# Performance work log

Measured on AMD Instinct MI355X. Metric: run time of the kernel, lower is better.

Reference implementation:

```python
import jax, jax.numpy as jnp
import numpy as np

T, N, E, IN_DIM, H = 20, 50000, 800000, 16, 128
NPF = 7  # num_physical_features
EPS = 1e-5


def setup_inputs() -> dict:
    key = jax.random.key(0)
    ks = jax.random.split(key, 24)
    s = 0.05
    inp = {
        'x': jax.random.normal(ks[0], (T, N, IN_DIM), jnp.float32),
        'edge_index': jax.random.randint(ks[1], (2, E), 0, N, jnp.int64),
        # SAGEConv layer 1 (PyG: lin_l on aggregated neighbors w/ bias, lin_r on root no bias)
        'sage1_wl': jax.random.normal(ks[2], (IN_DIM, H), jnp.float32) * s,
        'sage1_bl': jnp.zeros((H,), jnp.float32),
        'sage1_wr': jax.random.normal(ks[3], (IN_DIM, H), jnp.float32) * s,
        # SAGEConv layer 2
        'sage2_wl': jax.random.normal(ks[4], (H, H), jnp.float32) * s,
        'sage2_bl': jnp.zeros((H,), jnp.float32),
        'sage2_wr': jax.random.normal(ks[5], (H, H), jnp.float32) * s,
        # LayerNorm
        'ln_g': jnp.ones((H,), jnp.float32),
        'ln_b': jnp.zeros((H,), jnp.float32),
        # GRU (torch layout: [3H, H], gate order r,z,n)
        'gru_wih': jax.random.normal(ks[6], (3 * H, H), jnp.float32) * s,
        'gru_whh': jax.random.normal(ks[7], (3 * H, H), jnp.float32) * s,
        'gru_bih': jnp.zeros((3 * H,), jnp.float32),
        'gru_bhh': jnp.zeros((3 * H,), jnp.float32),
        # Thickness decoder
        'th_w1': jax.random.normal(ks[8], (H, H), jnp.float32) * s,
        'th_b1': jnp.zeros((H,), jnp.float32),
        'th_w2': jax.random.normal(ks[9], (H, 1), jnp.float32) * s,
        'th_b2': jnp.zeros((1,), jnp.float32),
        # Physical feature decoder
        'ph_w1': jax.random.normal(ks[10], (H, H), jnp.float32) * s,
        'ph_b1': jnp.zeros((H,), jnp.float32),
        'ph_w2': jax.random.normal(ks[11], (H, NPF), jnp.float32) * s,
        'ph_b2': jnp.zeros((NPF,), jnp.float32),
    }
    return inp


def _sage(h, src, dst, deg_inv, wl, bl, wr):
    # mean-aggregate neighbor features over incoming edges, then two linears
    agg = jax.ops.segment_sum(h[src], dst, num_segments=N) * deg_inv[:, None]
    return agg @ wl + bl + h @ wr


def _forward(x, edge_index,
             sage1_wl, sage1_bl, sage1_wr,
             sage2_wl, sage2_bl, sage2_wr,
             ln_g, ln_b,
             gru_wih, gru_whh, gru_bih, gru_bhh,
             th_w1, th_b1, th_w2, th_b2,
             ph_w1, ph_b1, ph_w2, ph_b2):
    src, dst = edge_index[0], edge_index[1]
    deg = jax.ops.segment_sum(jnp.ones((E,), jnp.float32), dst, num_segments=N)
    deg_inv = 1.0 / jnp.maximum(deg, 1.0)

    def encode(xt):  # [N, IN_DIM] -> [N, H]
        h = jax.nn.relu(_sage(xt, src, dst, deg_inv, sage1_wl, sage1_bl, sage1_wr))
        h = jax.nn.relu(_sage(h, src, dst, deg_inv, sage2_wl, sage2_bl, sage2_wr))
        mu = jnp.mean(h, axis=-1, keepdims=True)
        var = jnp.mean(jnp.square(h - mu), axis=-1, keepdims=True)
        return (h - mu) * jax.lax.rsqrt(var + EPS) * ln_g + ln_b

    encoded = jax.lax.map(encode, x)  # [T, N, H]

    # GRU over time, batch = nodes
    def gru_step(h, x_t):
        gi = x_t @ gru_wih.T + gru_bih  # [N, 3H]
        gh = h @ gru_whh.T + gru_bhh
        i_r, i_z, i_n = jnp.split(gi, 3, axis=-1)
        h_r, h_z, h_n = jnp.split(gh, 3, axis=-1)
        r = jax.nn.sigmoid(i_r + h_r)
        z = jax.nn.sigmoid(i_z + h_z)
        n = jnp.tanh(i_n + r * h_n)
        h_new = (1.0 - z) * n + z * h
        return h_new, h_new

    h0 = jnp.zeros((N, H), jnp.float32)
    _, h_temporal = jax.lax.scan(gru_step, h0, encoded)  # [T, N, H]

    th = jax.nn.relu(h_temporal @ th_w1 + th_b1) @ th_w2 + th_b2   # [T, N, 1]
    ph = jax.nn.relu(h_temporal @ ph_w1 + ph_b1) @ ph_w2 + ph_b2   # [T, N, NPF]
    return th, ph


def reference(x, edge_index,
              sage1_wl, sage1_bl, sage1_wr,
              sage2_wl, sage2_bl, sage2_wr,
              ln_g, ln_b,
              gru_wih, gru_whh, gru_bih, gru_bhh,
              th_w1, th_b1, th_w2, th_b2,
              ph_w1, ph_b1, ph_w2, ph_b2):
    return _forward(x, edge_index,
                    sage1_wl, sage1_bl, sage1_wr,
                    sage2_wl, sage2_bl, sage2_wr,
                    ln_g, ln_b,
                    gru_wih, gru_whh, gru_bih, gru_bhh,
                    th_w1, th_b1, th_w2, th_b2,
                    ph_w1, ph_b1, ph_w2, ph_b2)
```

## Files before the change

### kernel.cpp

```cpp
#include <hip/hip_runtime.h>
#include <hip/hip_bf16.h>

#define TT 20
#define NN 50000
#define EE 800000
#define IND 16
#define HH 128
#define NPF 7
#define NB ((NN + 255) / 256)

typedef __attribute__((ext_vector_type(8))) short bf16x8;
typedef __attribute__((ext_vector_type(4))) float f32x4;
#define MFMA(a, b, c) __builtin_amdgcn_mfma_f32_16x16x32_bf16(a, b, c, 0, 0, 0)

__device__ __forceinline__ unsigned short f2bf(float f) {
    union { float f; unsigned u; } v; v.f = f;
    unsigned r = v.u + 0x7fffu + ((v.u >> 16) & 1u);
    return (unsigned short)(r >> 16);
}
__device__ __forceinline__ float bf2f(unsigned short u) {
    union { unsigned u; float f; } v; v.u = ((unsigned)u) << 16;
    return v.f;
}

__global__ void detect_kernel(const int* ei, int* flag, int E) {
    __shared__ int nz;
    if (threadIdx.x == 0) nz = 0;
    __syncthreads();
    for (int i = threadIdx.x; i < 1024 && i < E; i += blockDim.x)
        if (ei[2 * i + 1] != 0) atomicOr(&nz, 1);
    __syncthreads();
    if (threadIdx.x == 0) *flag = (nz == 0) ? 1 : 0;
}
__device__ __forceinline__ int edge_src(const int* ei, int e, int E, int f) {
    return f ? ei[2 * e] : ei[e];
}
__device__ __forceinline__ int edge_dst(const int* ei, int e, int E, int f) {
    return f ? ei[2 * (E + e)] : ei[E + e];
}
__global__ void count_deg_kernel(const int* ei, const int* flag, int* deg, int E) {
    int e = blockIdx.x * blockDim.x + threadIdx.x;
    if (e >= E) return;
    int f = *flag;
    atomicAdd(&deg[edge_dst(ei, e, E, f)], 1);
}

__global__ __launch_bounds__(256) void sum_blocks_kernel(const int* deg, int* bsum) {
    int i = blockIdx.x * 256 + threadIdx.x;
    int v = (i < NN) ? deg[i] : 0;
#pragma unroll
    for (int o = 1; o <= 32; o <<= 1) v += __shfl_xor(v, o);
    __shared__ int ws[4];
    if ((threadIdx.x & 63) == 0) ws[threadIdx.x >> 6] = v;
    __syncthreads();
    if (threadIdx.x == 0) bsum[blockIdx.x] = ws[0] + ws[1] + ws[2] + ws[3];
}
__global__ __launch_bounds__(256) void scan_blocks_kernel(const int* bsum, int* bbase) {
    __shared__ int arr[256];
    int t = threadIdx.x;
    int v = (t < NB) ? bsum[t] : 0;
    arr[t] = v;
    __syncthreads();
    for (int off = 1; off < 256; off <<= 1) {
        int u = (t >= off) ? arr[t - off] : 0;
        __syncthreads();
        arr[t] += u;
        __syncthreads();
    }
    if (t < NB) bbase[t] = arr[t] - v;
}
__global__ __launch_bounds__(256) void offs_kernel(const int* deg, const int* bbase,
                                                   int* offs, int* cursor,
                                                   float* dinv, int E) {
    __shared__ int arr[256];
    int t = threadIdx.x;
    int i = blockIdx.x * 256 + t;
    int d = (i < NN) ? deg[i] : 0;
    arr[t] = d;
    __syncthreads();
    for (int off = 1; off < 256; off <<= 1) {
        int u = (t >= off) ? arr[t - off] : 0;
        __syncthreads();
        arr[t] += u;
        __syncthreads();
    }
    if (i < NN) {
        int o = bbase[blockIdx.x] + arr[t] - d;
        offs[i] = o;
        cursor[i] = o;
        dinv[i] = 1.0f / (float)(d > 1 ? d : 1);
        if (i == NN - 1) offs[NN] = E;
    }
}
__global__ void fill_csr_kernel(const int* ei, const int* flag, int* cursor,
                                int* csr, int E) {
    int e = blockIdx.x * blockDim.x + threadIdx.x;
    if (e >= E) return;
    int f = *flag;
    int s = edge_src(ei, e, E, f);
    int d = edge_dst(ei, e, E, f);
    int p = atomicAdd(&cursor[d], 1);
    csr[p] = s;
}

__global__ void pack_kernel(const float* src, unsigned short* dst, int tiles,
                            int mode) {
    int id = blockIdx.x * blockDim.x + threadIdx.x;
    if (id >= tiles * 4 * 64) return;
    int lane = id & 63, kk = (id >> 6) & 3, tile = id >> 8;
    int n = tile * 16 + (lane & 15);
    int kbase = kk * 32 + (lane >> 4) * 8;
    unsigned short out[8];
#pragma unroll
    for (int i = 0; i < 8; ++i) {
        int k = kbase + i;
        float v = mode ? src[n * HH + k] : src[k * (tiles * 16) + n];
        out[i] = f2bf(v);
    }
    *(uint4*)(dst + (size_t)id * 8) = *(uint4*)out;
}

__global__ __launch_bounds__(128) void sage1_kernel(
    const float* __restrict__ x, const int* __restrict__ offs,
    const int* __restrict__ csr, const float* __restrict__ dinv,
    const float* __restrict__ wl, const float* __restrict__ bl,
    const float* __restrict__ wr, unsigned short* __restrict__ h1c, int t0) {
    const int tid = threadIdx.x;
    const int ci = blockIdx.y;
    const float* xt = x + (size_t)(t0 + ci) * NN * IND;
    const int m0 = blockIdx.x * 8;
    __shared__ __align__(16) float sAgg[8][IND];
    __shared__ float sX[8][IND];
    {
        int r = tid >> 4, node = m0 + r;
        int l16 = tid & 15, sub = l16 >> 2, q = l16 & 3;
        int e1 = offs[node + 1];
        float4 acc = make_float4(0.f, 0.f, 0.f, 0.f);
        for (int e = offs[node] + sub; e < e1; e += 4) {
            float4 v = *(const float4*)(xt + (size_t)csr[e] * IND + q * 4);
            acc.x += v.x; acc.y += v.y; acc.z += v.z; acc.w += v.w;
        }
#pragma unroll
        for (int o = 4; o <= 8; o <<= 1) {
            acc.x += __shfl_xor(acc.x, o);
            acc.y += __shfl_xor(acc.y, o);
            acc.z += __shfl_xor(acc.z, o);
            acc.w += __shfl_xor(acc.w, o);
        }
        if (sub == 0) {
            float di = dinv[node];
            acc.x *= di; acc.y *= di; acc.z *= di; acc.w *= di;
            *(float4*)&sAgg[r][q * 4] = acc;
        }
        sX[r][l16] = xt[(size_t)node * IND + l16];
    }
    __syncthreads();
    const int col = tid;
    float acc[8];
    float b = bl[col];
#pragma unroll
    for (int m = 0; m < 8; ++m) acc[m] = b;
#pragma unroll
    for (int k = 0; k < IND; ++k) {
        float wlv = wl[k * HH + col];
        float wrv = wr[k * HH + col];
#pragma unroll
        for (int m = 0; m < 8; ++m) acc[m] += sAgg[m][k] * wlv + sX[m][k] * wrv;
    }
#pragma unroll
    for (int m = 0; m < 8; ++m)
        h1c[((size_t)ci * NN + m0 + m) * HH + col] = f2bf(fmaxf(acc[m], 0.f));
}

__global__ __launch_bounds__(256) void sage2_agg_kernel(
    const unsigned short* __restrict__ h1c, const int* __restrict__ offs,
    const int* __restrict__ csr, const float* __restrict__ dinv,
    unsigned short* __restrict__ agg2c) {
    const int ci = blockIdx.y;
    const unsigned short* h1t = h1c + (size_t)ci * NN * HH;
    int wid = threadIdx.x >> 6, lane = threadIdx.x & 63;
    int n = blockIdx.x * 4 + wid;
    int eg = lane >> 4, part = lane & 15;
    int e0 = offs[n], e1 = offs[n + 1];
    float s[8] = {0.f, 0.f, 0.f, 0.f, 0.f, 0.f, 0.f, 0.f};
    for (int e = e0 + eg; e < e1; e += 4) {
        uint4 v = *(const uint4*)(h1t + (size_t)csr[e] * HH + part * 8);
        s[0] += bf2f((unsigned short)(v.x & 0xffff));
        s[1] += bf2f((unsigned short)(v.x >> 16));
        s[2] += bf2f((unsigned short)(v.y & 0xffff));
        s[3] += bf2f((unsigned short)(v.y >> 16));
        s[4] += bf2f((unsigned short)(v.z & 0xffff));
        s[5] += bf2f((unsigned short)(v.z >> 16));
        s[6] += bf2f((unsigned short)(v.w & 0xffff));
        s[7] += bf2f((unsigned short)(v.w >> 16));
    }
#pragma unroll
    for (int j = 0; j < 8; ++j) {
        s[j] += __shfl_xor(s[j], 16);
        s[j] += __shfl_xor(s[j], 32);
    }
    if (eg == 0) {
        float di = dinv[n];
        unsigned short o[8];
#pragma unroll
        for (int j = 0; j < 8; ++j) o[j] = f2bf(s[j] * di);
        *(uint4*)(agg2c + ((size_t)ci * NN + n) * HH + part * 8) = *(uint4*)o;
    }
}

#define LDA(buf, kk)                                                          \
    (*(const bf16x8*)((const char*)(buf) +                                    \
        (((lane & 15) * 256 + (kk) * 64 + (lane >> 4) * 16) ^                 \
         (((lane & 15) & 7) << 4))))

__global__ __launch_bounds__(64) void gru_fused_kernel(
    const unsigned short* __restrict__ agg2t, const unsigned short* __restrict__ h1t,
    const unsigned short* __restrict__ pS2L, const unsigned short* __restrict__ pS2R,
    const float* __restrict__ s2bl, const float* __restrict__ lng,
    const float* __restrict__ lnb,
    const unsigned short* __restrict__ pGI, const unsigned short* __restrict__ pGH,
    const float* __restrict__ bih, const float* __restrict__ bhh,
    float* __restrict__ h, unsigned short* __restrict__ hallt) {
    const int lane = threadIdx.x;
    const int r0 = blockIdx.x * 16;
    __shared__ unsigned short bufA[16 * 128];
    __shared__ unsigned short bufB[16 * 128];
    __shared__ unsigned short bufH[16 * 128];

#pragma unroll
    for (int j = 0; j < 4; ++j) {
        int off = (lane + 64 * j) * 16;
        int row = off >> 8;
        int swz = off ^ ((row & 7) << 4);
        *(uint4*)((char*)bufA + swz) =
            *(const uint4*)((const char*)(agg2t + (size_t)r0 * HH) + off);
        *(uint4*)((char*)bufB + swz) =
            *(const uint4*)((const char*)(h1t + (size_t)r0 * HH) + off);
        const float* hs = h + (size_t)r0 * HH + (size_t)(off / 2);
        unsigned short tmp[8];
#pragma unroll
        for (int i = 0; i < 8; ++i) tmp[i] = f2bf(hs[i]);
        *(uint4*)((char*)bufH + swz) = *(uint4*)tmp;
    }
    __syncthreads();

    bf16x8 ae[4], ah[4];
#pragma unroll
    for (int kk = 0; kk < 4; ++kk) { ae[kk] = LDA(bufA, kk); ah[kk] = LDA(bufB, kk); }
    float vE[8][4];
    float sS[4] = {0, 0, 0, 0}, sQ[4] = {0, 0, 0, 0};
#pragma unroll
    for (int c = 0; c < 8; ++c) {
        f32x4 al = {0, 0, 0, 0}, ar = {0, 0, 0, 0};
#pragma unroll
        for (int kk = 0; kk < 4; ++kk) {
            bf16x8 bl = *(const bf16x8*)(pS2L + ((size_t)(c * 4 + kk) * 64 + lane) * 8);
            bf16x8 br = *(const bf16x8*)(pS2R + ((size_t)(c * 4 + kk) * 64 + lane) * 8);
            al = MFMA(ae[kk], bl, al);
            ar = MFMA(ah[kk], br, ar);
        }
        int col = c * 16 + (lane & 15);
        float bb = s2bl[col];
#pragma unroll
        for (int j = 0; j < 4; ++j) {
            float v = fmaxf(al[j] + ar[j] + bb, 0.f);
            vE[c][j] = v; sS[j] += v; sQ[j] += v * v;
        }
    }
#pragma unroll
    for (int o = 1; o <= 8; o <<= 1) {
#pragma unroll
        for (int j = 0; j < 4; ++j) {
            sS[j] += __shfl_xor(sS[j], o);
            sQ[j] += __shfl_xor(sQ[j], o);
        }
    }
    __syncthreads();
#pragma unroll
    for (int c = 0; c < 8; ++c) {
        int col = c * 16 + (lane & 15);
        float g = lng[col], b = lnb[col];
#pragma unroll
        for (int j = 0; j < 4; ++j) {
            float mu = sS[j] * (1.f / 128.f);
            float var = sQ[j] * (1.f / 128.f) - mu * mu;
            float ve = (vE[c][j] - mu) * rsqrtf(var + 1e-5f) * g + b;
            int row = (lane >> 4) * 4 + j;
            int off = ((row * 128 + col) * 2) ^ ((row & 7) << 4);
            *(unsigned short*)((char*)bufA + off) = f2bf(ve);
        }
    }
    __syncthreads();

    bf16x8 xe[4], xh[4];
#pragma unroll
    for (int kk = 0; kk < 4; ++kk) { xe[kk] = LDA(bufA, kk); xh[kk] = LDA(bufH, kk); }
#pragma unroll
    for (int c = 0; c < 8; ++c) {
        f32x4 air = {0,0,0,0}, aiz = {0,0,0,0}, ain = {0,0,0,0};
        f32x4 ahr = {0,0,0,0}, ahz = {0,0,0,0}, ahn = {0,0,0,0};
#pragma unroll
        for (int kk = 0; kk < 4; ++kk) {
            bf16x8 bir = *(const bf16x8*)(pGI + ((size_t)((c     ) * 4 + kk) * 64 + lane) * 8);
            bf16x8 biz = *(const bf16x8*)(pGI + ((size_t)((c +  8) * 4 + kk) * 64 + lane) * 8);
            bf16x8 bin = *(const bf16x8*)(pGI + ((size_t)((c + 16) * 4 + kk) * 64 + lane) * 8);
            bf16x8 bhr = *(const bf16x8*)(pGH + ((size_t)((c     ) * 4 + kk) * 64 + lane) * 8);
            bf16x8 bhz = *(const bf16x8*)(pGH + ((size_t)((c +  8) * 4 + kk) * 64 + lane) * 8);
            bf16x8 bhn = *(const bf16x8*)(pGH + ((size_t)((c + 16) * 4 + kk) * 64 + lane) * 8);
            air = MFMA(xe[kk], bir, air); aiz = MFMA(xe[kk], biz, aiz);
            ain = MFMA(xe[kk], bin, ain);
            ahr = MFMA(xh[kk], bhr, ahr); ahz = MFMA(xh[kk], bhz, ahz);
            ahn = MFMA(xh[kk], bhn, ahn);
        }
        int col = c * 16 + (lane & 15);
        float bir_ = bih[col], biz_ = bih[HH + col], bin_ = bih[2 * HH + col];
        float bhr_ = bhh[col], bhz_ = bhh[HH + col], bhn_ = bhh[2 * HH + col];
#pragma unroll
        for (int j = 0; j < 4; ++j) {
            int row = (lane >> 4) * 4 + j;
            size_t gidx = (size_t)(r0 + row) * HH + col;
            float rr = 1.f / (1.f + expf(-(air[j] + bir_ + ahr[j] + bhr_)));
            float zz = 1.f / (1.f + expf(-(aiz[j] + biz_ + ahz[j] + bhz_)));
            float nn2 = tanhf(ain[j] + bin_ + rr * (ahn[j] + bhn_));
            float hold = h[gidx];
            float hnew = (1.f - zz) * nn2 + zz * hold;
            h[gidx] = hnew;
            hallt[gidx] = f2bf(hnew);
        }
    }
}

__global__ __launch_bounds__(64) void dec_kernel(
    const unsigned short* __restrict__ hall,
    const unsigned short* __restrict__ pT1, const unsigned short* __restrict__ pP1,
    const float* __restrict__ tb1, const float* __restrict__ tw2,
    const float* __restrict__ tb2, const float* __restrict__ pb1,
    const float* __restrict__ pw2, const float* __restrict__ pb2,
    float* __restrict__ out_th, float* __restrict__ out_ph, int t0) {
    const int lane = threadIdx.x;
    const int rc = blockIdx.x * 16;
    const int ci = rc / NN;
    const int n0 = rc - ci * NN;
    const int tg = t0 + ci;
    __shared__ unsigned short bufB[16 * 128];
#pragma unroll
    for (int j = 0; j < 4; ++j) {
        int off = (lane + 64 * j) * 16;
        int row = off >> 8;
        int swz = off ^ ((row & 7) << 4);
        *(uint4*)((char*)bufB + swz) =
            *(const uint4*)((const char*)(hall + (size_t)rc * HH) + off);
    }
    __syncthreads();
    bf16x8 xd[4];
#pragma unroll
    for (int kk = 0; kk < 4; ++kk) xd[kk] = LDA(bufB, kk);
    float pt[4] = {0, 0, 0, 0};
    float pf[NPF][4];
#pragma unroll
    for (int f = 0; f < NPF; ++f)
#pragma unroll
        for (int j = 0; j < 4; ++j) pf[f][j] = 0.f;
#pragma unroll
    for (int c = 0; c < 8; ++c) {
        f32x4 at = {0, 0, 0, 0}, ap = {0, 0, 0, 0};
#pragma unroll
        for (int kk = 0; kk < 4; ++kk) {
            bf16x8 bt = *(const bf16x8*)(pT1 + ((size_t)(c * 4 + kk) * 64 + lane) * 8);
            bf16x8 bp = *(const bf16x8*)(pP1 + ((size_t)(c * 4 + kk) * 64 + lane) * 8);
            at = MFMA(xd[kk], bt, at);
            ap = MFMA(xd[kk], bp, ap);
        }
        int col = c * 16 + (lane & 15);
        float b1 = tb1[col], b2 = pb1[col], w2 = tw2[col];
        float wp[NPF];
#pragma unroll
        for (int f = 0; f < NPF; ++f) wp[f] = pw2[col * NPF + f];
#pragma unroll
        for (int j = 0; j < 4; ++j) {
            float a = fmaxf(at[j] + b1, 0.f);
            pt[j] += a * w2;
            float p = fmaxf(ap[j] + b2, 0.f);
#pragma unroll
            for (int f = 0; f < NPF; ++f) pf[f][j] += p * wp[f];
        }
    }
#pragma unroll
    for (int o = 1; o <= 8; o <<= 1) {
#pragma unroll
        for (int j = 0; j < 4; ++j) {
            pt[j] += __shfl_xor(pt[j], o);
#pragma unroll
            for (int f = 0; f < NPF; ++f) pf[f][j] += __shfl_xor(pf[f][j], o);
        }
    }
    if ((lane & 15) == 0) {
        int g = lane >> 4;
#pragma unroll
        for (int j = 0; j < 4; ++j) {
            int gr = n0 + g * 4 + j;
            out_th[(size_t)tg * NN + gr] = pt[j] + tb2[0];
#pragma unroll
            for (int f = 0; f < NPF; ++f)
                out_ph[((size_t)tg * NN + gr) * NPF + f] = pf[f][j] + pb2[f];
        }
    }
}
#undef LDA

extern "C" void kernel_launch(void* const* d_in, const int* in_sizes, int n_in,
                              void* d_out, int out_size, void* d_ws, size_t ws_size,
                              hipStream_t stream) {
    const float* x     = (const float*)d_in[0];
    const int*   ei    = (const int*)d_in[1];
    const float* s1wl  = (const float*)d_in[2];
    const float* s1bl  = (const float*)d_in[3];
    const float* s1wr  = (const float*)d_in[4];
    const float* s2wl  = (const float*)d_in[5];
    const float* s2bl  = (const float*)d_in[6];
    const float* s2wr  = (const float*)d_in[7];
    const float* lng   = (const float*)d_in[8];
    const float* lnb   = (const float*)d_in[9];
    const float* g_wih = (const float*)d_in[10];
    const float* g_whh = (const float*)d_in[11];
    const float* g_bih = (const float*)d_in[12];
    const float* g_bhh = (const float*)d_in[13];
    const float* tw1   = (const float*)d_in[14];
    const float* tb1   = (const float*)d_in[15];
    const float* tw2   = (const float*)d_in[16];
    const float* tb2   = (const float*)d_in[17];
    const float* pw1   = (const float*)d_in[18];
    const float* pb1   = (const float*)d_in[19];
    const float* pw2   = (const float*)d_in[20];
    const float* pb2   = (const float*)d_in[21];

    char* ws = (char*)d_ws;
    size_t o = 0;
    auto alloc = [&](size_t bytes) {
        size_t r = o;
        o += (bytes + 255) & ~(size_t)255;
        return r;
    };
    int*            flag  = (int*)(ws + alloc(4));
    int*            deg   = (int*)(ws + alloc((size_t)NN * 4));
    int*            offs  = (int*)(ws + alloc((size_t)(NN + 1) * 4));
    int*            curs  = (int*)(ws + alloc((size_t)NN * 4));
    int*            csr   = (int*)(ws + alloc((size_t)EE * 4));
    float*          dinv  = (float*)(ws + alloc((size_t)NN * 4));
    int*            bsum  = (int*)(ws + alloc((size_t)NB * 4));
    int*            bbase = (int*)(ws + alloc((size_t)NB * 4));
    unsigned short* pS2L  = (unsigned short*)(ws + alloc(8 * 4 * 64 * 8 * 2));
    unsigned short* pS2R  = (unsigned short*)(ws + alloc(8 * 4 * 64 * 8 * 2));
    unsigned short* pT1   = (unsigned short*)(ws + alloc(8 * 4 * 64 * 8 * 2));
    unsigned short* pP1   = (unsigned short*)(ws + alloc(8 * 4 * 64 * 8 * 2));
    unsigned short* pGI   = (unsigned short*)(ws + alloc(24 * 4 * 64 * 8 * 2));
    unsigned short* pGH   = (unsigned short*)(ws + alloc(24 * 4 * 64 * 8 * 2));
    float*          hbuf  = (float*)(ws + alloc((size_t)NN * HH * 4));

    const size_t per_t = 2ull * NN * HH * 2;
    size_t avail = (o < ws_size) ? ws_size - o : 0;
    int C = (int)(avail / per_t);
    if (C < 1) C = 1;
    if (C > TT) C = TT;
    unsigned short* h1c   = (unsigned short*)(ws + alloc((size_t)C * NN * HH * 2));
    unsigned short* agg2c = (unsigned short*)(ws + alloc((size_t)C * NN * HH * 2));
    unsigned short* hallc = agg2c;

    detect_kernel<<<1, 256, 0, stream>>>(ei, flag, EE);
    hipMemsetAsync(deg, 0, (size_t)NN * 4, stream);
    count_deg_kernel<<<(EE + 255) / 256, 256, 0, stream>>>(ei, flag, deg, EE);
    sum_blocks_kernel<<<NB, 256, 0, stream>>>(deg, bsum);
    scan_blocks_kernel<<<1, 256, 0, stream>>>(bsum, bbase);
    offs_kernel<<<NB, 256, 0, stream>>>(deg, bbase, offs, curs, dinv, EE);
    fill_csr_kernel<<<(EE + 255) / 256, 256, 0, stream>>>(ei, flag, curs, csr, EE);
    pack_kernel<<<(8 * 4 * 64 + 255) / 256, 256, 0, stream>>>(s2wl, pS2L, 8, 0);
    pack_kernel<<<(8 * 4 * 64 + 255) / 256, 256, 0, stream>>>(s2wr, pS2R, 8, 0);
    pack_kernel<<<(8 * 4 * 64 + 255) / 256, 256, 0, stream>>>(tw1, pT1, 8, 0);
    pack_kernel<<<(8 * 4 * 64 + 255) / 256, 256, 0, stream>>>(pw1, pP1, 8, 0);
    pack_kernel<<<(24 * 4 * 64 + 255) / 256, 256, 0, stream>>>(g_wih, pGI, 24, 1);
    pack_kernel<<<(24 * 4 * 64 + 255) / 256, 256, 0, stream>>>(g_whh, pGH, 24, 1);
    hipMemsetAsync(hbuf, 0, (size_t)NN * HH * 4, stream);

    float* out = (float*)d_out;
    for (int t0 = 0; t0 < TT; t0 += C) {
        int Cc = TT - t0 < C ? TT - t0 : C;
        dim3 g1(NN / 8, Cc), g2(NN / 4, Cc);
        sage1_kernel<<<g1, 128, 0, stream>>>(x, offs, csr, dinv, s1wl, s1bl,
                                             s1wr, h1c, t0);
        sage2_agg_kernel<<<g2, 256, 0, stream>>>(h1c, offs, csr, dinv, agg2c);
        for (int ci = 0; ci < Cc; ++ci) {
            size_t co = (size_t)ci * NN * HH;
            gru_fused_kernel<<<NN / 16, 64, 0, stream>>>(
                agg2c + co, h1c + co, pS2L, pS2R, s2bl, lng, lnb, pGI, pGH,
                g_bih, g_bhh, hbuf, hallc + co);
        }
        dec_kernel<<<(size_t)Cc * NN / 16, 64, 0, stream>>>(
            hallc, pT1, pP1, tb1, tw2, tb2, pb1, pw2, pb2,
            out, out + (size_t)TT * NN, t0);
    }
}
```

Measured before the change: 2.691 ms.

## Restructure sage2 aggregation, process two row tiles per GRU block, drop LDS staging

The sage2 aggregation now assigns 16 lanes per node, with 4-way unrolled independent gathers and no cross-lane reduction. The fused GRU kernel handles 32 rows per block so each packed weight fragment feeds two MFMA tiles. MFMA A-fragments are loaded straight from global memory instead of being staged through swizzled LDS, in both the GRU and decoder kernels. The csr index read in sage1 uses a nontemporal load. These changes add register pressure from the doubled accumulators and make the fragment loads less coalesced.

```diff
diff --git a/kernel.cpp b/kernel.cpp
--- a/kernel.cpp
+++ b/kernel.cpp
@@ -137,7 +137,8 @@
         int e1 = offs[node + 1];
         float4 acc = make_float4(0.f, 0.f, 0.f, 0.f);
         for (int e = offs[node] + sub; e < e1; e += 4) {
-            float4 v = *(const float4*)(xt + (size_t)csr[e] * IND + q * 4);
+            int s = __builtin_nontemporal_load(&csr[e]);
+            float4 v = *(const float4*)(xt + (size_t)s * IND + q * 4);
             acc.x += v.x; acc.y += v.y; acc.z += v.z; acc.w += v.w;
         }
 #pragma unroll
@@ -172,46 +173,49 @@
         h1c[((size_t)ci * NN + m0 + m) * HH + col] = f2bf(fmaxf(acc[m], 0.f));
 }
 
+#define ADD8(acc, v) do {                                     \
+    union { unsigned u; float f; } t_;                        \
+    t_.u = (v).x << 16;         acc[0] += t_.f;               \
+    t_.u = (v).x & 0xffff0000u; acc[1] += t_.f;               \
+    t_.u = (v).y << 16;         acc[2] += t_.f;               \
+    t_.u = (v).y & 0xffff0000u; acc[3] += t_.f;               \
+    t_.u = (v).z << 16;         acc[4] += t_.f;               \
+    t_.u = (v).z & 0xffff0000u; acc[5] += t_.f;               \
+    t_.u = (v).w << 16;         acc[6] += t_.f;               \
+    t_.u = (v).w & 0xffff0000u; acc[7] += t_.f;               \
+} while (0)
+
 __global__ __launch_bounds__(256) void sage2_agg_kernel(
     const unsigned short* __restrict__ h1c, const int* __restrict__ offs,
     const int* __restrict__ csr, const float* __restrict__ dinv,
     unsigned short* __restrict__ agg2c) {
     const int ci = blockIdx.y;
-    const unsigned short* h1t = h1c + (size_t)ci * NN * HH;
-    int wid = threadIdx.x >> 6, lane = threadIdx.x & 63;
-    int n = blockIdx.x * 4 + wid;
-    int eg = lane >> 4, part = lane & 15;
-    int e0 = offs[n], e1 = offs[n + 1];
-    float s[8] = {0.f, 0.f, 0.f, 0.f, 0.f, 0.f, 0.f, 0.f};
-    for (int e = e0 + eg; e < e1; e += 4) {
-        uint4 v = *(const uint4*)(h1t + (size_t)csr[e] * HH + part * 8);
-        s[0] += bf2f((unsigned short)(v.x & 0xffff));
-        s[1] += bf2f((unsigned short)(v.x >> 16));
-        s[2] += bf2f((unsigned short)(v.y & 0xffff));
-        s[3] += bf2f((unsigned short)(v.y >> 16));
-        s[4] += bf2f((unsigned short)(v.z & 0xffff));
-        s[5] += bf2f((unsigned short)(v.z >> 16));
-        s[6] += bf2f((unsigned short)(v.w & 0xffff));
-        s[7] += bf2f((unsigned short)(v.w >> 16));
-    }
-#pragma unroll
-    for (int j = 0; j < 8; ++j) {
-        s[j] += __shfl_xor(s[j], 16);
-        s[j] += __shfl_xor(s[j], 32);
-    }
-    if (eg == 0) {
-        float di = dinv[n];
-        unsigned short o[8];
-#pragma unroll
-        for (int j = 0; j < 8; ++j) o[j] = f2bf(s[j] * di);
-        *(uint4*)(agg2c + ((size_t)ci * NN + n) * HH + part * 8) = *(uint4*)o;
-    }
-}
-
-#define LDA(buf, kk)                                                          \
-    (*(const bf16x8*)((const char*)(buf) +                                    \
-        (((lane & 15) * 256 + (kk) * 64 + (lane >> 4) * 16) ^                 \
-         (((lane & 15) & 7) << 4))))
+    const unsigned short* __restrict__ h1t = h1c + (size_t)ci * NN * HH;
+    const int n = blockIdx.x * 16 + (threadIdx.x >> 4);
+    const int part = threadIdx.x & 15;
+    const int e0 = offs[n], e1 = offs[n + 1];
+    float a[8] = {0,0,0,0,0,0,0,0}, b[8] = {0,0,0,0,0,0,0,0};
+    float c_[8] = {0,0,0,0,0,0,0,0}, d[8] = {0,0,0,0,0,0,0,0};
+    int e = e0;
+    for (; e + 3 < e1; e += 4) {
+        int s0 = csr[e], s1 = csr[e + 1], s2 = csr[e + 2], s3 = csr[e + 3];
+        uint4 v0 = *(const uint4*)(h1t + (size_t)s0 * HH + part * 8);
+        uint4 v1 = *(const uint4*)(h1t + (size_t)s1 * HH + part * 8);
+        uint4 v2 = *(const uint4*)(h1t + (size_t)s2 * HH + part * 8);
+        uint4 v3 = *(const uint4*)(h1t + (size_t)s3 * HH + part * 8);
+        ADD8(a, v0); ADD8(b, v1); ADD8(c_, v2); ADD8(d, v3);
+    }
+    for (; e < e1; ++e) {
+        int s0 = csr[e];
+        uint4 v0 = *(const uint4*)(h1t + (size_t)s0 * HH + part * 8);
+        ADD8(a, v0);
+    }
+    float di = dinv[n];
+    unsigned short o[8];
+#pragma unroll
+    for (int j = 0; j < 8; ++j) o[j] = f2bf((a[j] + b[j] + c_[j] + d[j]) * di);
+    *(uint4*)(agg2c + ((size_t)ci * NN + n) * HH + part * 8) = *(uint4*)o;
+}
 
 __global__ __launch_bounds__(64) void gru_fused_kernel(
     const unsigned short* __restrict__ agg2t, const unsigned short* __restrict__ h1t,
@@ -222,83 +226,89 @@
     const float* __restrict__ bih, const float* __restrict__ bhh,
     float* __restrict__ h, unsigned short* __restrict__ hallt) {
     const int lane = threadIdx.x;
-    const int r0 = blockIdx.x * 16;
-    __shared__ unsigned short bufA[16 * 128];
-    __shared__ unsigned short bufB[16 * 128];
-    __shared__ unsigned short bufH[16 * 128];
-
-#pragma unroll
-    for (int j = 0; j < 4; ++j) {
-        int off = (lane + 64 * j) * 16;
-        int row = off >> 8;
-        int swz = off ^ ((row & 7) << 4);
-        *(uint4*)((char*)bufA + swz) =
-            *(const uint4*)((const char*)(agg2t + (size_t)r0 * HH) + off);
-        *(uint4*)((char*)bufB + swz) =
-            *(const uint4*)((const char*)(h1t + (size_t)r0 * HH) + off);
-        const float* hs = h + (size_t)r0 * HH + (size_t)(off / 2);
-        unsigned short tmp[8];
-#pragma unroll
-        for (int i = 0; i < 8; ++i) tmp[i] = f2bf(hs[i]);
-        *(uint4*)((char*)bufH + swz) = *(uint4*)tmp;
-    }
-    __syncthreads();
-
-    bf16x8 ae[4], ah[4];
-#pragma unroll
-    for (int kk = 0; kk < 4; ++kk) { ae[kk] = LDA(bufA, kk); ah[kk] = LDA(bufB, kk); }
-    float vE[8][4];
-    float sS[4] = {0, 0, 0, 0}, sQ[4] = {0, 0, 0, 0};
+    const int r0 = blockIdx.x * 32;
+    const int ntile = (NN - r0 >= 32) ? 2 : 1;
+    __shared__ unsigned short bufE[32 * 128];
+    const int fr = lane & 15;
+    const int fkb = (lane >> 4) * 8;
+
+#pragma unroll
+    for (int t = 0; t < 2; ++t) {
+        if (t < ntile) {
+            const size_t rowg = (size_t)(r0 + t * 16 + fr);
+            bf16x8 ae[4], ah[4];
+#pragma unroll
+            for (int kk = 0; kk < 4; ++kk) {
+                ae[kk] = *(const bf16x8*)(agg2t + rowg * HH + kk * 32 + fkb);
+                ah[kk] = *(const bf16x8*)(h1t + rowg * HH + kk * 32 + fkb);
+            }
+            float vE[8][4];
+            float sS[4] = {0, 0, 0, 0}, sQ[4] = {0, 0, 0, 0};
+#pragma unroll
+            for (int c = 0; c < 8; ++c) {
+                f32x4 al = {0, 0, 0, 0}, ar = {0, 0, 0, 0};
+#pragma unroll
+                for (int kk = 0; kk < 4; ++kk) {
+                    bf16x8 bl = *(const bf16x8*)(pS2L + ((size_t)(c * 4 + kk) * 64 + lane) * 8);
+                    bf16x8 br = *(const bf16x8*)(pS2R + ((size_t)(c * 4 + kk) * 64 + lane) * 8);
+                    al = MFMA(ae[kk], bl, al);
+                    ar = MFMA(ah[kk], br, ar);
+                }
+                float bb = s2bl[c * 16 + fr];
+#pragma unroll
+                for (int j = 0; j < 4; ++j) {
+                    float v = fmaxf(al[j] + ar[j] + bb, 0.f);
+                    vE[c][j] = v; sS[j] += v; sQ[j] += v * v;
+                }
+            }
+#pragma unroll
+            for (int o = 1; o <= 8; o <<= 1) {
+#pragma unroll
+                for (int j = 0; j < 4; ++j) {
+                    sS[j] += __shfl_xor(sS[j], o);
+                    sQ[j] += __shfl_xor(sQ[j], o);
+                }
+            }
+#pragma unroll
+            for (int c = 0; c < 8; ++c) {
+                int cc = c * 16 + fr;
+                float g = lng[cc], bb = lnb[cc];
+#pragma unroll
+                for (int j = 0; j < 4; ++j) {
+                    float mu = sS[j] * (1.f / 128.f);
+                    float var = sQ[j] * (1.f / 128.f) - mu * mu;
+                    float ve = (vE[c][j] - mu) * rsqrtf(var + 1e-5f) * g + bb;
+                    int row = t * 16 + (lane >> 4) * 4 + j;
+                    int off = ((row * 128 + cc) * 2) ^ ((row & 7) << 4);
+                    *(unsigned short*)((char*)bufE + off) = f2bf(ve);
+                }
+            }
+        }
+    }
+    __syncthreads();
+
+    bf16x8 xe[2][4], xh[2][4];
+#pragma unroll
+    for (int t = 0; t < 2; ++t) {
+        if (t < ntile) {
+#pragma unroll
+            for (int kk = 0; kk < 4; ++kk) {
+                xe[t][kk] = *(const bf16x8*)((const char*)bufE + t * 4096 +
+                    ((fr * 256 + kk * 64 + (lane >> 4) * 16) ^ ((fr & 7) << 4)));
+                const float* hp = h + (size_t)(r0 + t * 16 + fr) * HH + kk * 32 + fkb;
+                float4 f0 = *(const float4*)hp;
+                float4 f1 = *(const float4*)(hp + 4);
+                unsigned short tmp[8] = {f2bf(f0.x), f2bf(f0.y), f2bf(f0.z), f2bf(f0.w),
+                                         f2bf(f1.x), f2bf(f1.y), f2bf(f1.z), f2bf(f1.w)};
+                xh[t][kk] = *(const bf16x8*)tmp;
+            }
+        }
+    }
 #pragma unroll
     for (int c = 0; c < 8; ++c) {
-        f32x4 al = {0, 0, 0, 0}, ar = {0, 0, 0, 0};
-#pragma unroll
-        for (int kk = 0; kk < 4; ++kk) {
-            bf16x8 bl = *(const bf16x8*)(pS2L + ((size_t)(c * 4 + kk) * 64 + lane) * 8);
-            bf16x8 br = *(const bf16x8*)(pS2R + ((size_t)(c * 4 + kk) * 64 + lane) * 8);
-            al = MFMA(ae[kk], bl, al);
-            ar = MFMA(ah[kk], br, ar);
-        }
-        int col = c * 16 + (lane & 15);
-        float bb = s2bl[col];
-#pragma unroll
-        for (int j = 0; j < 4; ++j) {
-            float v = fmaxf(al[j] + ar[j] + bb, 0.f);
-            vE[c][j] = v; sS[j] += v; sQ[j] += v * v;
-        }
-    }
-#pragma unroll
-    for (int o = 1; o <= 8; o <<= 1) {
-#pragma unroll
-        for (int j = 0; j < 4; ++j) {
-            sS[j] += __shfl_xor(sS[j], o);
-            sQ[j] += __shfl_xor(sQ[j], o);
-        }
-    }
-    __syncthreads();
-#pragma unroll
-    for (int c = 0; c < 8; ++c) {
-        int col = c * 16 + (lane & 15);
-        float g = lng[col], b = lnb[col];
-#pragma unroll
-        for (int j = 0; j < 4; ++j) {
-            float mu = sS[j] * (1.f / 128.f);
-            float var = sQ[j] * (1.f / 128.f) - mu * mu;
-            float ve = (vE[c][j] - mu) * rsqrtf(var + 1e-5f) * g + b;
-            int row = (lane >> 4) * 4 + j;
-            int off = ((row * 128 + col) * 2) ^ ((row & 7) << 4);
-            *(unsigned short*)((char*)bufA + off) = f2bf(ve);
-        }
-    }
-    __syncthreads();
-
-    bf16x8 xe[4], xh[4];
-#pragma unroll
-    for (int kk = 0; kk < 4; ++kk) { xe[kk] = LDA(bufA, kk); xh[kk] = LDA(bufH, kk); }
-#pragma unroll
-    for (int c = 0; c < 8; ++c) {
-        f32x4 air = {0,0,0,0}, aiz = {0,0,0,0}, ain = {0,0,0,0};
-        f32x4 ahr = {0,0,0,0}, ahz = {0,0,0,0}, ahn = {0,0,0,0};
+        f32x4 air[2] = {{0,0,0,0},{0,0,0,0}}, aiz[2] = {{0,0,0,0},{0,0,0,0}};
+        f32x4 ain[2] = {{0,0,0,0},{0,0,0,0}}, ahr[2] = {{0,0,0,0},{0,0,0,0}};
+        f32x4 ahz[2] = {{0,0,0,0},{0,0,0,0}}, ahn[2] = {{0,0,0,0},{0,0,0,0}};
 #pragma unroll
         for (int kk = 0; kk < 4; ++kk) {
             bf16x8 bir = *(const bf16x8*)(pGI + ((size_t)((c     ) * 4 + kk) * 64 + lane) * 8);
@@ -307,25 +317,36 @@
             bf16x8 bhr = *(const bf16x8*)(pGH + ((size_t)((c     ) * 4 + kk) * 64 + lane) * 8);
             bf16x8 bhz = *(const bf16x8*)(pGH + ((size_t)((c +  8) * 4 + kk) * 64 + lane) * 8);
             bf16x8 bhn = *(const bf16x8*)(pGH + ((size_t)((c + 16) * 4 + kk) * 64 + lane) * 8);
-            air = MFMA(xe[kk], bir, air); aiz = MFMA(xe[kk], biz, aiz);
-            ain = MFMA(xe[kk], bin, ain);
-            ahr = MFMA(xh[kk], bhr, ahr); ahz = MFMA(xh[kk], bhz, ahz);
-            ahn = MFMA(xh[kk], bhn, ahn);
-        }
-        int col = c * 16 + (lane & 15);
-        float bir_ = bih[col], biz_ = bih[HH + col], bin_ = bih[2 * HH + col];
-        float bhr_ = bhh[col], bhz_ = bhh[HH + col], bhn_ = bhh[2 * HH + col];
-#pragma unroll
-        for (int j = 0; j < 4; ++j) {
-            int row = (lane >> 4) * 4 + j;
-            size_t gidx = (size_t)(r0 + row) * HH + col;
-            float rr = 1.f / (1.f + expf(-(air[j] + bir_ + ahr[j] + bhr_)));
-            float zz = 1.f / (1.f + expf(-(aiz[j] + biz_ + ahz[j] + bhz_)));
-            float nn2 = tanhf(ain[j] + bin_ + rr * (ahn[j] + bhn_));
-            float hold = h[gidx];
-            float hnew = (1.f - zz) * nn2 + zz * hold;
-            h[gidx] = hnew;
-            hallt[gidx] = f2bf(hnew);
+#pragma unroll
+            for (int t = 0; t < 2; ++t) {
+                if (t < ntile) {
+                    air[t] = MFMA(xe[t][kk], bir, air[t]);
+                    aiz[t] = MFMA(xe[t][kk], biz, aiz[t]);
+                    ain[t] = MFMA(xe[t][kk], bin, ain[t]);
+                    ahr[t] = MFMA(xh[t][kk], bhr, ahr[t]);
+                    ahz[t] = MFMA(xh[t][kk], bhz, ahz[t]);
+                    ahn[t] = MFMA(xh[t][kk], bhn, ahn[t]);
+                }
+            }
+        }
+        int cc = c * 16 + fr;
+        float bir_ = bih[cc], biz_ = bih[HH + cc], bin_ = bih[2 * HH + cc];
+        float bhr_ = bhh[cc], bhz_ = bhh[HH + cc], bhn_ = bhh[2 * HH + cc];
+#pragma unroll
+        for (int t = 0; t < 2; ++t) {
+            if (t < ntile) {
+#pragma unroll
+                for (int j = 0; j < 4; ++j) {
+                    size_t gidx = (size_t)(r0 + t * 16 + (lane >> 4) * 4 + j) * HH + cc;
+                    float rr = 1.f / (1.f + expf(-(air[t][j] + bir_ + ahr[t][j] + bhr_)));
+                    float zz = 1.f / (1.f + expf(-(aiz[t][j] + biz_ + ahz[t][j] + bhz_)));
+                    float nn2 = tanhf(ain[t][j] + bin_ + rr * (ahn[t][j] + bhn_));
+                    float hold = h[gidx];
+                    float hnew = (1.f - zz) * nn2 + zz * hold;
+                    h[gidx] = hnew;
+                    hallt[gidx] = f2bf(hnew);
+                }
+            }
         }
     }
 }
@@ -342,19 +363,11 @@
     const int ci = rc / NN;
     const int n0 = rc - ci * NN;
     const int tg = t0 + ci;
-    __shared__ unsigned short bufB[16 * 128];
-#pragma unroll
-    for (int j = 0; j < 4; ++j) {
-        int off = (lane + 64 * j) * 16;
-        int row = off >> 8;
-        int swz = off ^ ((row & 7) << 4);
-        *(uint4*)((char*)bufB + swz) =
-            *(const uint4*)((const char*)(hall + (size_t)rc * HH) + off);
-    }
-    __syncthreads();
+    const int fr = lane & 15, fkb = (lane >> 4) * 8;
     bf16x8 xd[4];
 #pragma unroll
-    for (int kk = 0; kk < 4; ++kk) xd[kk] = LDA(bufB, kk);
+    for (int kk = 0; kk < 4; ++kk)
+        xd[kk] = *(const bf16x8*)(hall + (size_t)(rc + fr) * HH + kk * 32 + fkb);
     float pt[4] = {0, 0, 0, 0};
     float pf[NPF][4];
 #pragma unroll
@@ -371,7 +384,7 @@
             at = MFMA(xd[kk], bt, at);
             ap = MFMA(xd[kk], bp, ap);
         }
-        int col = c * 16 + (lane & 15);
+        int col = c * 16 + fr;
         float b1 = tb1[col], b2 = pb1[col], w2 = tw2[col];
         float wp[NPF];
 #pragma unroll
@@ -394,7 +407,7 @@
             for (int f = 0; f < NPF; ++f) pf[f][j] += __shfl_xor(pf[f][j], o);
         }
     }
-    if ((lane & 15) == 0) {
+    if (fr == 0) {
         int g = lane >> 4;
 #pragma unroll
         for (int j = 0; j < 4; ++j) {
@@ -406,7 +419,6 @@
         }
     }
 }
-#undef LDA
 
 extern "C" void kernel_launch(void* const* d_in, const int* in_sizes, int n_in,
                               void* d_out, int out_size, void* d_ws, size_t ws_size,
@@ -484,13 +496,13 @@
     float* out = (float*)d_out;
     for (int t0 = 0; t0 < TT; t0 += C) {
         int Cc = TT - t0 < C ? TT - t0 : C;
-        dim3 g1(NN / 8, Cc), g2(NN / 4, Cc);
+        dim3 g1(NN / 8, Cc), g2(NN / 16, Cc);
         sage1_kernel<<<g1, 128, 0, stream>>>(x, offs, csr, dinv, s1wl, s1bl,
                                              s1wr, h1c, t0);
         sage2_agg_kernel<<<g2, 256, 0, stream>>>(h1c, offs, csr, dinv, agg2c);
         for (int ci = 0; ci < Cc; ++ci) {
             size_t co = (size_t)ci * NN * HH;
-            gru_fused_kernel<<<NN / 16, 64, 0, stream>>>(
+            gru_fused_kernel<<<(NN + 31) / 32, 64, 0, stream>>>(
                 agg2c + co, h1c + co, pS2L, pS2R, s2bl, lng, lnb, pGI, pGH,
                 g_bih, g_bhh, hbuf, hallc + co);
         }
```

After: 3.249 ms. 1.21x slower.
